# Kernel tuning notes

Hardware: AMD Instinct MI355X
Metric: run time of the kernel (lower is better)

The kernel has to match this reference:

```python
import jax, jax.numpy as jnp
import numpy as np

B = 8192      # env batch
M = 16        # n_machine
HID = 128     # machine_hidden_dim
HEADS = 1
BN_EPS = 1e-5


def _gat(h, gat_W, gat_a):
    # h: (B2, 2, HID); gat_W: (HID, HEADS*HID); gat_a: (HEADS, 2*HID, 1)
    B2 = h.shape[0]
    Wh = (h @ gat_W).reshape(B2, 2, HEADS, HID).transpose(0, 2, 1, 3)  # (B2,H,2,hid)
    src = jnp.einsum('bhnf,hfo->bhno', Wh, gat_a[:, :HID, :])   # (B2,H,2,1)
    tgt = jnp.einsum('bhnf,hfo->bhno', Wh, gat_a[:, HID:, :])   # (B2,H,2,1)
    e = jax.nn.leaky_relu(src + jnp.swapaxes(tgt, -1, -2), negative_slope=0.2)  # (B2,H,2,2)
    # static adjacency: row0 attends to both nodes, row1 only to itself (2->1 directed)
    adj = jnp.array([[1.0, 1.0], [0.0, 1.0]], dtype=e.dtype)
    e = jnp.where(adj > 0, e, jnp.asarray(-9e15, e.dtype))
    att = jax.nn.softmax(e, axis=-1)
    h_prime = att @ Wh                 # (B2,H,2,hid)
    return h_prime.mean(axis=1)        # concat=False -> mean over heads -> (B2,2,hid)


def setup_inputs() -> dict:
    key = jax.random.key(0)
    ks = jax.random.split(key, 24)
    s = 0.05
    inp = {
        'machine_fea_1': jax.random.normal(ks[0], (B, M, 6), jnp.float32),
        'machine_fea_2': jax.random.normal(ks[1], (B, M, 8), jnp.float32),
        'h_pooled_o': jax.random.normal(ks[2], (B, HID), jnp.float32),
        'machine_mask': jnp.zeros((B, 1, M), dtype=bool),
        # params (Linear weights stored as (in, out); original Linears have bias=False for feature projections)
        'W1': jax.random.normal(ks[3], (6, HID), jnp.float32) * s,
        'W2': jax.random.normal(ks[4], (8, HID), jnp.float32) * s,
        'gat_W': jax.random.normal(ks[5], (HID, HEADS * HID), jnp.float32) * s,
        'gat_a': jax.random.normal(ks[6], (HEADS, 2 * HID, 1), jnp.float32) * s,
        'bn_gamma': jnp.ones((HID,), jnp.float32),
        'bn_beta': jnp.zeros((HID,), jnp.float32),
        # MLPActor: 3 layers, in=3*HID, hidden=HID, out=1 (tanh hidden, linear out)
        'Wa1': jax.random.normal(ks[7], (3 * HID, HID), jnp.float32) * s,
        'ba1': jnp.zeros((HID,), jnp.float32),
        'Wa2': jax.random.normal(ks[8], (HID, HID), jnp.float32) * s,
        'ba2': jnp.zeros((HID,), jnp.float32),
        'Wa3': jax.random.normal(ks[9], (HID, 1), jnp.float32) * s,
        'ba3': jnp.zeros((1,), jnp.float32),
        # MLPCritic: 3 layers, in=HID, hidden=HID, out=2
        'Wc1': jax.random.normal(ks[10], (HID, HID), jnp.float32) * s,
        'bc1': jnp.zeros((HID,), jnp.float32),
        'Wc2': jax.random.normal(ks[11], (HID, HID), jnp.float32) * s,
        'bc2': jnp.zeros((HID,), jnp.float32),
        'Wc3': jax.random.normal(ks[12], (HID, 2), jnp.float32) * s,
        'bc3': jnp.zeros((2,), jnp.float32),
    }
    return inp


def reference(machine_fea_1, machine_fea_2, h_pooled_o, machine_mask,
              W1, W2, gat_W, gat_a, bn_gamma, bn_beta,
              Wa1, ba1, Wa2, ba2, Wa3, ba3,
              Wc1, bc1, Wc2, bc2, Wc3, bc3):
    m_fea1 = machine_fea_1 @ W1                       # (B,M,HID)
    m_fea2 = machine_fea_2 @ W2                       # (B,M,HID)
    # pair the two projections per machine node: (B*M, 2, HID)
    h12 = jnp.stack([m_fea1.reshape(-1, HID), m_fea2.reshape(-1, HID)], axis=1)
    g = jax.nn.elu(_gat(h12, gat_W, gat_a))
    g = jax.nn.elu(_gat(g, gat_W, gat_a))
    g = _gat(g, gat_W, gat_a)
    # NOTE: h_machine_feas is computed but unused downstream in the original forward (ablation)
    h_machine_feas = g.mean(axis=-2).reshape(-1, M, HID)
    # BatchNorm1d in training mode over flattened (B*M, HID)
    flat = m_fea1.reshape(-1, HID)
    mu = flat.mean(axis=0)
    var = flat.var(axis=0)  # biased, as torch BN uses for normalization
    h_m_nodes = (((flat - mu) / jnp.sqrt(var + BN_EPS)) * bn_gamma + bn_beta).reshape(-1, M, HID)
    h_pooled = h_m_nodes.mean(axis=1)                 # (B,HID)
    concat = jnp.concatenate([
        h_m_nodes,
        jnp.broadcast_to(h_pooled[:, None, :], h_m_nodes.shape),
        jnp.broadcast_to(h_pooled_o[:, None, :], h_m_nodes.shape),
    ], axis=-1)                                       # (B,M,3*HID)
    x = jnp.tanh(concat @ Wa1 + ba1)
    x = jnp.tanh(x @ Wa2 + ba2)
    mch_scores = (x @ Wa3 + ba3).squeeze(-1) * 10.0   # (B,M)
    mask = machine_mask.squeeze(1)
    mch_scores = jnp.where(mask, -jnp.inf, mch_scores)
    mch_prob = jax.nn.softmax(mch_scores, axis=-1)
    v = jnp.tanh(h_pooled @ Wc1 + bc1)
    v = jnp.tanh(v @ Wc2 + bc2)
    machine_v = v @ Wc3 + bc3                         # (B,2)
    return (mch_prob, h_pooled, machine_v)
```

## Files before the change

### kernel.cpp

```cpp
#include <hip/hip_runtime.h>
#include <hip/hip_bf16.h>
#include <math.h>

#define HID    128
#define BATCH  8192
#define NM     16
#define NROWS  (BATCH * NM)
#define BN_EPS 1e-5f

#define S1_BLOCKS   256
#define S1_ROWS     (NROWS / S1_BLOCKS)
#define PREP_BLOCKS 32
#define TOT_BLOCKS  (S1_BLOCKS + PREP_BLOCKS)

#define WS_PART  0
#define WS_SCALE 8192
#define WS_SHIFT 8320
#define WS_M1    8448
#define WS_SV    9216
#define WS_N1    9344
#define WS_CV    10112
#define WS_BW    10240

#define O1 ((size_t)BATCH * NM)
#define O2 (O1 + (size_t)BATCH * HID)

#define G    4
#define ROWS (G * NM)
#define LDH  136
#define ZLD  136
#define LDV  132

typedef __attribute__((ext_vector_type(8))) short short8_t;
typedef __attribute__((ext_vector_type(4))) float f32x4;

#define MFMA16(a, b, c) __builtin_amdgcn_mfma_f32_16x16x32_bf16(a, b, c, 0, 0, 0)

__device__ __forceinline__ unsigned short f2bf(float x) {
    __hip_bfloat16 h = __float2bfloat16(x);
    return *reinterpret_cast<unsigned short*>(&h);
}
__device__ __forceinline__ float bf2f(unsigned short u) {
    __hip_bfloat16 h = *reinterpret_cast<__hip_bfloat16*>(&u);
    return __bfloat162float(h);
}
__device__ __forceinline__ float ftanh(float x) {
    float e = __expf(2.0f * x);
    return 1.0f - 2.0f / (e + 1.0f);
}

__global__ __launch_bounds__(512) void stats_prep_kernel(
    const float* __restrict__ fea1,
    const float* __restrict__ Wa1, const float* __restrict__ Wa2,
    const float* __restrict__ Wc2,
    float* __restrict__ ws, unsigned short* __restrict__ wbt)
{
    const int tid = threadIdx.x;
    const int blk = blockIdx.x;

    if (blk >= S1_BLOCKS) {
        const int idx = (blk - S1_BLOCKS) * 512 + tid;
        const int k = idx >> 7, c = idx & 127;
        wbt[c * 128 + k]         = f2bf(Wa1[idx]);
        wbt[16384 + c * 128 + k] = f2bf(Wa2[idx]);
        wbt[32768 + c * 128 + k] = f2bf(Wa1[32768 + idx]);
        wbt[49152 + c * 128 + k] = f2bf(Wc2[idx]);
        return;
    }

    __shared__ float feaS[S1_ROWS * 6];
    __shared__ float redM[8 * 27];

    const float* src = fea1 + (size_t)blk * (S1_ROWS * 6);
    for (int i = tid; i < S1_ROWS * 6; i += 512) feaS[i] = src[i];
    __syncthreads();

    float f[6];
    #pragma unroll
    for (int j = 0; j < 6; ++j) f[j] = feaS[tid * 6 + j];

    float acc[27];
    #pragma unroll
    for (int j = 0; j < 6; ++j) acc[j] = f[j];
    {
        int idx = 6;
        #pragma unroll
        for (int j = 0; j < 6; ++j)
            #pragma unroll
            for (int k = j; k < 6; ++k) acc[idx++] = f[j] * f[k];
    }
    #pragma unroll
    for (int j = 0; j < 27; ++j) {
        acc[j] += __shfl_xor(acc[j], 1);
        acc[j] += __shfl_xor(acc[j], 2);
        acc[j] += __shfl_xor(acc[j], 4);
        acc[j] += __shfl_xor(acc[j], 8);
        acc[j] += __shfl_xor(acc[j], 16);
        acc[j] += __shfl_xor(acc[j], 32);
    }
    const int wv = tid >> 6;
    if ((tid & 63) == 0) {
        #pragma unroll
        for (int j = 0; j < 27; ++j) redM[wv * 27 + j] = acc[j];
    }
    __syncthreads();
    if (tid < 27) {
        float s = 0.f;
        #pragma unroll
        for (int w2 = 0; w2 < 8; ++w2) s += redM[w2 * 27 + tid];
        ws[WS_PART + blk * 32 + tid] = s;
    }
}

__global__ __launch_bounds__(512) void finalize_kernel(
    const float* __restrict__ W1,  const float* __restrict__ Wa1,
    const float* __restrict__ Wc1, const float* __restrict__ bc1,
    const float* __restrict__ gamma, const float* __restrict__ beta,
    float* __restrict__ ws, unsigned short* __restrict__ wbt)
{
    __shared__ float stageA[128 * 128];
    __shared__ float stageC[128 * 128];
    __shared__ double momS[27];
    __shared__ float scS2[HID], shS[HID];
    __shared__ float w1sS[6 * HID];

    const int tid = threadIdx.x;

    for (int i = tid; i < 128 * 128; i += 512) {
        stageA[i] = Wa1[16384 + i];
        stageC[i] = Wc1[i];
    }

    {
        const int j = tid >> 4;
        const int l = tid & 15;
        double s = 0.0;
        if (j < 27)
            for (int p = l; p < S1_BLOCKS; p += 16)
                s += (double)ws[WS_PART + p * 32 + j];
        s += __shfl_xor(s, 1);
        s += __shfl_xor(s, 2);
        s += __shfl_xor(s, 4);
        s += __shfl_xor(s, 8);
        if (j < 27 && l == 0) momS[j] = s;
    }
    __syncthreads();

    if (tid < 128) {
        float wv[6];
        #pragma unroll
        for (int j = 0; j < 6; ++j) wv[j] = W1[j * HID + tid];
        double sum = 0.0, ssq = 0.0;
        #pragma unroll
        for (int j = 0; j < 6; ++j) sum += (double)wv[j] * momS[j];
        {
            int idx = 6;
            #pragma unroll
            for (int j = 0; j < 6; ++j)
                #pragma unroll
                for (int k = j; k < 6; ++k) {
                    double t = (double)wv[j] * (double)wv[k] * momS[idx++];
                    ssq += (j == k) ? t : 2.0 * t;
                }
        }
        const double inv = 1.0 / (double)NROWS;
        double mu  = sum * inv;
        double var = ssq * inv - mu * mu;
        float sc = gamma[tid] * rsqrtf((float)var + BN_EPS);
        float sh = beta[tid] - (float)mu * sc;
        ws[WS_SCALE + tid] = sc;
        ws[WS_SHIFT + tid] = sh;
        scS2[tid] = sc;
        shS[tid]  = sh;
    }
    __syncthreads();
    for (int i = tid; i < 6 * HID; i += 512)
        w1sS[i] = W1[i] * scS2[i & 127];
    __syncthreads();

    if (tid < 256) {
        const int cc = tid & 127;
        const float* st = (tid < 128) ? stageA : stageC;
        float a[7] = {0.f, 0.f, 0.f, 0.f, 0.f, 0.f, 0.f};
        for (int k = 0; k < HID; ++k) {
            const float sv = st[k * 128 + cc];
            #pragma unroll
            for (int j = 0; j < 6; ++j)
                a[j] += w1sS[j * HID + k] * sv;
            a[6] += shS[k] * sv;
        }
        if (tid < 128) {
            #pragma unroll
            for (int j = 0; j < 6; ++j) ws[WS_M1 + j * HID + cc] = a[j];
            ws[WS_SV + cc] = a[6];
        } else {
            #pragma unroll
            for (int j = 0; j < 6; ++j) ws[WS_N1 + j * HID + cc] = a[j];
            ws[WS_CV + cc] = a[6] + bc1[cc];
        }
    }

    for (int idx = tid; idx < HID * 32; idx += 512) {
        const int col = idx >> 5, k = idx & 31;
        unsigned short v = 0;
        int kr = -1; bool lo = false;
        if (k < 6)                    kr = k;
        else if (k >= 8  && k < 14)   kr = k - 8;
        else if (k >= 16 && k < 22) { kr = k - 16; lo = true; }
        if (kr >= 0) {
            const float wv = w1sS[kr * HID + col];
            const unsigned short hi = f2bf(wv);
            v = lo ? f2bf(wv - bf2f(hi)) : hi;
        }
        wbt[65536 + col * 32 + k] = v;
    }
}

__global__ __launch_bounds__(256, 4) void main_kernel(
    const float* __restrict__ fea1, const float* __restrict__ hpo,
    const unsigned char* __restrict__ mask,
    const float* __restrict__ W1,
    const float* __restrict__ ba1, const float* __restrict__ ba2,
    const float* __restrict__ Wa3, const float* __restrict__ ba3,
    const float* __restrict__ bc2,
    const float* __restrict__ Wc3, const float* __restrict__ bc3,
    const float* __restrict__ ws, const unsigned short* __restrict__ wbt,
    float* __restrict__ out)
{
    __shared__ __align__(16) unsigned short hmS[ROWS * LDH];
    __shared__ __align__(16) unsigned short x1S[ROWS * LDH];
    __shared__ __align__(16) unsigned short zS[G * ZLD];
    __shared__ __align__(16) unsigned short v1bS[4 * LDV];
    __shared__ __align__(16) unsigned short v2bS[4 * LDV];
    __shared__ float scS[4 * ROWS];
    __shared__ float fmS[4][8];

    float* feaS = (float*)x1S;

    const int tid = threadIdx.x;
    const int b0  = blockIdx.x * G;

    const int w    = tid >> 6;
    const int lane = tid & 63;
    const int lr   = lane & 15;
    const int lg   = lane >> 4;
    const int n0   = 2 * w;

    const unsigned short* wbt1  = wbt;
    const unsigned short* wbt2  = wbt + 16384;
    const unsigned short* wbtB  = wbt + 32768;
    const unsigned short* wbtC2 = wbt + 49152;
    const unsigned short* wbtW1 = wbt + 65536;

    for (int i = tid; i < ROWS * 6; i += 256) feaS[i] = fea1[(size_t)b0 * (NM * 6) + i];
    for (int i = tid; i < G * HID; i += 256) {
        const int g = i >> 7, cc = i & 127;
        zS[g * ZLD + cc] = f2bf(hpo[(size_t)b0 * HID + i]);
    }

    short8_t bW[2];
    #pragma unroll
    for (int t = 0; t < 2; ++t)
        bW[t] = *(const short8_t*)(wbtW1 + ((n0 + t) * 16 + lr) * 32 + lg * 8);
    short8_t b1f[2][4];
    #pragma unroll
    for (int t = 0; t < 2; ++t) {
        const unsigned short* br = wbt1 + ((n0 + t) * 16 + lr) * 128 + lg * 8;
        #pragma unroll
        for (int kk = 0; kk < 4; ++kk) b1f[t][kk] = *(const short8_t*)(br + kk * 32);
    }
    const float sh0 = ws[WS_SHIFT + n0 * 16 + lr];
    const float sh1 = ws[WS_SHIFT + (n0 + 1) * 16 + lr];
    __syncthreads();

    #pragma unroll
    for (int g = 0; g < 4; ++g) {
        const float* fr = feaS + (g * 16 + lr) * 6;
        short8_t af;
        #pragma unroll
        for (int j = 0; j < 6; ++j) {
            const float x = fr[j];
            const unsigned short hx = f2bf(x);
            const unsigned short lx = f2bf(x - bf2f(hx));
            unsigned short sel = (lg == 1) ? lx : hx;
            if (lg == 3) sel = 0;
            af[j] = (short)sel;
        }
        af[6] = 0; af[7] = 0;

        #pragma unroll
        for (int t = 0; t < 2; ++t) {
            const float sh = t ? sh1 : sh0;
            f32x4 acc = {sh, sh, sh, sh};
            acc = MFMA16(af, bW[t], acc);
            #pragma unroll
            for (int i = 0; i < 4; ++i)
                hmS[(g * 16 + lg * 4 + i) * LDH + (n0 + t) * 16 + lr] = f2bf(acc[i]);
        }
    }
    if (tid < 24) {
        const int g = tid / 6, j = tid % 6;
        float s = 0.f;
        for (int m = 0; m < NM; ++m) s += feaS[(g * 16 + m) * 6 + j];
        fmS[g][j] = s * (1.0f / NM);
    }
    __syncthreads();

    f32x4 accB[2];
    {
        short8_t bBf[2][4];
        #pragma unroll
        for (int t = 0; t < 2; ++t) {
            const unsigned short* br = wbtB + ((n0 + t) * 16 + lr) * 128 + lg * 8;
            #pragma unroll
            for (int kk = 0; kk < 4; ++kk) bBf[t][kk] = *(const short8_t*)(br + kk * 32);
        }
        short8_t za[4];
        const unsigned short* zr = zS + (lr & 3) * ZLD + lg * 8;
        #pragma unroll
        for (int kk = 0; kk < 4; ++kk) za[kk] = *(const short8_t*)(zr + kk * 32);

        float fm[4][6];
        #pragma unroll
        for (int g = 0; g < 4; ++g)
            #pragma unroll
            for (int j = 0; j < 6; ++j) fm[g][j] = fmS[g][j];

        #pragma unroll
        for (int t = 0; t < 2; ++t) {
            const int col = (n0 + t) * 16 + lr;
            const float bias = ba1[col] + ws[WS_SV + col];
            float b_[4];
            #pragma unroll
            for (int g = 0; g < 4; ++g) {
                float a = bias;
                #pragma unroll
                for (int j = 0; j < 6; ++j) a += fm[g][j] * ws[WS_M1 + j * HID + col];
                b_[g] = a;
            }
            f32x4 acc = {b_[0], b_[1], b_[2], b_[3]};
            acc = MFMA16(za[0], bBf[t][0], acc);
            acc = MFMA16(za[1], bBf[t][1], acc);
            acc = MFMA16(za[2], bBf[t][2], acc);
            acc = MFMA16(za[3], bBf[t][3], acc);
            accB[t] = acc;
        }

        #pragma unroll
        for (int t = 0; t < 2; ++t) {
            const int col = (n0 + t) * 16 + lr;
            float a = ws[WS_CV + col];
            #pragma unroll
            for (int j = 0; j < 6; ++j) a += fm[lg][j] * ws[WS_N1 + j * HID + col];
            v1bS[lg * LDV + col] = f2bf(ftanh(a));
        }

        #pragma unroll
        for (int t = 0; t < 2; ++t) {
            const int col = (n0 + t) * 16 + lr;
            float a = 0.f;
            #pragma unroll
            for (int j = 0; j < 6; ++j) a += fm[lg][j] * W1[j * HID + col];
            a = a * ws[WS_SCALE + col] + ws[WS_SHIFT + col];
            out[O1 + (size_t)(b0 + lg) * HID + col] = a;
        }
    }

    short8_t b2f[2][4];
    #pragma unroll
    for (int t = 0; t < 2; ++t) {
        const unsigned short* br = wbt2 + ((n0 + t) * 16 + lr) * 128 + lg * 8;
        #pragma unroll
        for (int kk = 0; kk < 4; ++kk) b2f[t][kk] = *(const short8_t*)(br + kk * 32);
    }

    #pragma unroll
    for (int g = 0; g < 4; ++g) {
        short8_t ha[4];
        const unsigned short* ar = hmS + (g * 16 + lr) * LDH + lg * 8;
        #pragma unroll
        for (int kk = 0; kk < 4; ++kk) ha[kk] = *(const short8_t*)(ar + kk * 32);
        #pragma unroll
        for (int t = 0; t < 2; ++t) {
            const float bz = accB[t][g];
            f32x4 acc = {bz, bz, bz, bz};
            acc = MFMA16(ha[0], b1f[t][0], acc);
            acc = MFMA16(ha[1], b1f[t][1], acc);
            acc = MFMA16(ha[2], b1f[t][2], acc);
            acc = MFMA16(ha[3], b1f[t][3], acc);
            #pragma unroll
            for (int i = 0; i < 4; ++i)
                x1S[(g * 16 + lg * 4 + i) * LDH + (n0 + t) * 16 + lr] = f2bf(ftanh(acc[i]));
        }
    }
    __syncthreads();

    {
        short8_t va[4];
        const unsigned short* vr = v1bS + (lr & 3) * LDV + lg * 8;
        #pragma unroll
        for (int kk = 0; kk < 4; ++kk) va[kk] = *(const short8_t*)(vr + kk * 32);
        #pragma unroll
        for (int t = 0; t < 2; ++t) {
            const int n = n0 + t;
            const unsigned short* br = wbtC2 + (n * 16 + lr) * 128 + lg * 8;
            const float bi = bc2[n * 16 + lr];
            f32x4 acc = {bi, bi, bi, bi};
            acc = MFMA16(va[0], *(const short8_t*)(br),      acc);
            acc = MFMA16(va[1], *(const short8_t*)(br + 32), acc);
            acc = MFMA16(va[2], *(const short8_t*)(br + 64), acc);
            acc = MFMA16(va[3], *(const short8_t*)(br + 96), acc);
            if (lg == 0) {
                #pragma unroll
                for (int i = 0; i < 4; ++i)
                    v2bS[i * LDV + n * 16 + lr] = f2bf(ftanh(acc[i]));
            }
        }

        float p[4][4];
        #pragma unroll
        for (int g = 0; g < 4; ++g)
            #pragma unroll
            for (int i = 0; i < 4; ++i) p[g][i] = 0.f;

        const float wv0 = Wa3[n0 * 16 + lr];
        const float wv1 = Wa3[(n0 + 1) * 16 + lr];
        const float bi0 = ba2[n0 * 16 + lr];
        const float bi1 = ba2[(n0 + 1) * 16 + lr];
        #pragma unroll
        for (int g = 0; g < 4; ++g) {
            short8_t ha[4];
            const unsigned short* ar = x1S + (g * 16 + lr) * LDH + lg * 8;
            #pragma unroll
            for (int kk = 0; kk < 4; ++kk) ha[kk] = *(const short8_t*)(ar + kk * 32);
            #pragma unroll
            for (int t = 0; t < 2; ++t) {
                const float bi = t ? bi1 : bi0;
                f32x4 acc = {bi, bi, bi, bi};
                acc = MFMA16(ha[0], b2f[t][0], acc);
                acc = MFMA16(ha[1], b2f[t][1], acc);
                acc = MFMA16(ha[2], b2f[t][2], acc);
                acc = MFMA16(ha[3], b2f[t][3], acc);
                const float wv = t ? wv1 : wv0;
                #pragma unroll
                for (int i = 0; i < 4; ++i)
                    p[g][i] += ftanh(acc[i]) * wv;
            }
        }
        #pragma unroll
        for (int g = 0; g < 4; ++g) {
            #pragma unroll
            for (int i = 0; i < 4; ++i) {
                float v = p[g][i];
                v += __shfl_xor(v, 1);
                v += __shfl_xor(v, 2);
                v += __shfl_xor(v, 4);
                v += __shfl_xor(v, 8);
                if (lr == 0) scS[w * ROWS + g * 16 + lg * 4 + i] = v;
            }
        }
    }
    __syncthreads();

    {
        const int g = w;
        float s = scS[0 * ROWS + g * 16 + lr] + scS[1 * ROWS + g * 16 + lr]
                + scS[2 * ROWS + g * 16 + lr] + scS[3 * ROWS + g * 16 + lr];
        s = (s + ba3[0]) * 10.0f;
        if (mask[(size_t)(b0 + g) * NM + lr]) s = -INFINITY;
        float mx = s;
        mx = fmaxf(mx, __shfl_xor(mx, 1));
        mx = fmaxf(mx, __shfl_xor(mx, 2));
        mx = fmaxf(mx, __shfl_xor(mx, 4));
        mx = fmaxf(mx, __shfl_xor(mx, 8));
        float e = __expf(s - mx);
        float sum = e;
        sum += __shfl_xor(sum, 1);
        sum += __shfl_xor(sum, 2);
        sum += __shfl_xor(sum, 4);
        sum += __shfl_xor(sum, 8);
        if (lane < NM)
            out[(size_t)(b0 + g) * NM + lr] = e / sum;
    }

    {
        const int g = w;
        const int k2 = lane * 2;
        float v0 = bf2f(v2bS[g * LDV + k2]);
        float v1 = bf2f(v2bS[g * LDV + k2 + 1]);
        float4 wc = *(const float4*)(Wc3 + k2 * 2);
        float p0 = v0 * wc.x + v1 * wc.z;
        float p1 = v0 * wc.y + v1 * wc.w;
        p0 += __shfl_xor(p0, 1);  p1 += __shfl_xor(p1, 1);
        p0 += __shfl_xor(p0, 2);  p1 += __shfl_xor(p1, 2);
        p0 += __shfl_xor(p0, 4);  p1 += __shfl_xor(p1, 4);
        p0 += __shfl_xor(p0, 8);  p1 += __shfl_xor(p1, 8);
        p0 += __shfl_xor(p0, 16); p1 += __shfl_xor(p1, 16);
        p0 += __shfl_xor(p0, 32); p1 += __shfl_xor(p1, 32);
        if (lane == 0) {
            out[O2 + (size_t)(b0 + g) * 2 + 0] = p0 + bc3[0];
            out[O2 + (size_t)(b0 + g) * 2 + 1] = p1 + bc3[1];
        }
    }
}

extern "C" void kernel_launch(void* const* d_in, const int* in_sizes, int n_in,
                              void* d_out, int out_size, void* d_ws, size_t ws_size,
                              hipStream_t stream)
{
    const float* fea1  = (const float*)d_in[0];
    const float* hpo   = (const float*)d_in[2];
    const unsigned char* mask = (const unsigned char*)d_in[3];
    const float* W1    = (const float*)d_in[4];
    const float* gamma = (const float*)d_in[8];
    const float* beta  = (const float*)d_in[9];
    const float* Wa1   = (const float*)d_in[10];
    const float* ba1   = (const float*)d_in[11];
    const float* Wa2   = (const float*)d_in[12];
    const float* ba2   = (const float*)d_in[13];
    const float* Wa3   = (const float*)d_in[14];
    const float* ba3   = (const float*)d_in[15];
    const float* Wc1   = (const float*)d_in[16];
    const float* bc1   = (const float*)d_in[17];
    const float* Wc2   = (const float*)d_in[18];
    const float* bc2   = (const float*)d_in[19];
    const float* Wc3   = (const float*)d_in[20];
    const float* bc3   = (const float*)d_in[21];

    float* ws = (float*)d_ws;
    unsigned short* wbt = (unsigned short*)(ws + WS_BW);
    float* out = (float*)d_out;

    stats_prep_kernel<<<TOT_BLOCKS, 512, 0, stream>>>(
        fea1, Wa1, Wa2, Wc2, ws, wbt);
    finalize_kernel<<<1, 512, 0, stream>>>(
        W1, Wa1, Wc1, bc1, gamma, beta, ws, wbt);
    main_kernel<<<BATCH / G, 256, 0, stream>>>(
        fea1, hpo, mask, W1, ba1, ba2, Wa3, ba3,
        bc2, Wc3, bc3, ws, wbt, out);
}
```

Measured before the change: 73.67 us.

## Split finalize kernel across three blocks with K-split weight folding

The single-block finalize kernel becomes three blocks. Block 0 folds the BN scale into the Wa1 slice, block 1 folds it into Wc1, and block 2 builds the bf16 W1 tile. The weight folding now reads global memory directly and splits the K dimension over four thread groups, with partial sums reduced in shared memory, so the large 128KB shared staging buffers and the idle threads are gone. The cost is that every block redoes the moment reduction and BN statistics.

```diff
diff --git a/kernel.cpp b/kernel.cpp
--- a/kernel.cpp
+++ b/kernel.cpp
@@ -118,18 +118,13 @@
     const float* __restrict__ gamma, const float* __restrict__ beta,
     float* __restrict__ ws, unsigned short* __restrict__ wbt)
 {
-    __shared__ float stageA[128 * 128];
-    __shared__ float stageC[128 * 128];
     __shared__ double momS[27];
     __shared__ float scS2[HID], shS[HID];
     __shared__ float w1sS[6 * HID];
+    __shared__ float partS[4 * 7 * HID];
 
     const int tid = threadIdx.x;
-
-    for (int i = tid; i < 128 * 128; i += 512) {
-        stageA[i] = Wa1[16384 + i];
-        stageC[i] = Wc1[i];
-    }
+    const int blk = blockIdx.x;
 
     {
         const int j = tid >> 4;
@@ -168,51 +163,68 @@
         double var = ssq * inv - mu * mu;
         float sc = gamma[tid] * rsqrtf((float)var + BN_EPS);
         float sh = beta[tid] - (float)mu * sc;
-        ws[WS_SCALE + tid] = sc;
-        ws[WS_SHIFT + tid] = sh;
         scS2[tid] = sc;
         shS[tid]  = sh;
+        if (blk == 0) {
+            ws[WS_SCALE + tid] = sc;
+            ws[WS_SHIFT + tid] = sh;
+        }
     }
     __syncthreads();
     for (int i = tid; i < 6 * HID; i += 512)
         w1sS[i] = W1[i] * scS2[i & 127];
     __syncthreads();
 
-    if (tid < 256) {
+    if (blk == 2) {
+        for (int idx = tid; idx < HID * 32; idx += 512) {
+            const int col = idx >> 5, k = idx & 31;
+            unsigned short v = 0;
+            int kr = -1; bool lo = false;
+            if (k < 6)                    kr = k;
+            else if (k >= 8  && k < 14)   kr = k - 8;
+            else if (k >= 16 && k < 22) { kr = k - 16; lo = true; }
+            if (kr >= 0) {
+                const float wv = w1sS[kr * HID + col];
+                const unsigned short hi = f2bf(wv);
+                v = lo ? f2bf(wv - bf2f(hi)) : hi;
+            }
+            wbt[65536 + col * 32 + k] = v;
+        }
+        return;
+    }
+
+    {
+        const float* st = (blk == 0) ? (Wa1 + 16384) : Wc1;
         const int cc = tid & 127;
-        const float* st = (tid < 128) ? stageA : stageC;
+        const int kq = tid >> 7;
         float a[7] = {0.f, 0.f, 0.f, 0.f, 0.f, 0.f, 0.f};
-        for (int k = 0; k < HID; ++k) {
+        for (int k = kq * 32; k < kq * 32 + 32; ++k) {
             const float sv = st[k * 128 + cc];
             #pragma unroll
             for (int j = 0; j < 6; ++j)
                 a[j] += w1sS[j * HID + k] * sv;
             a[6] += shS[k] * sv;
         }
-        if (tid < 128) {
-            #pragma unroll
-            for (int j = 0; j < 6; ++j) ws[WS_M1 + j * HID + cc] = a[j];
-            ws[WS_SV + cc] = a[6];
-        } else {
-            #pragma unroll
-            for (int j = 0; j < 6; ++j) ws[WS_N1 + j * HID + cc] = a[j];
-            ws[WS_CV + cc] = a[6] + bc1[cc];
-        }
-    }
-
-    for (int idx = tid; idx < HID * 32; idx += 512) {
-        const int col = idx >> 5, k = idx & 31;
-        unsigned short v = 0;
-        int kr = -1; bool lo = false;
-        if (k < 6)                    kr = k;
-        else if (k >= 8  && k < 14)   kr = k - 8;
-        else if (k >= 16 && k < 22) { kr = k - 16; lo = true; }
-        if (kr >= 0) {
-            const float wv = w1sS[kr * HID + col];
-            const unsigned short hi = f2bf(wv);
-            v = lo ? f2bf(wv - bf2f(hi)) : hi;
-        }
-        wbt[65536 + col * 32 + k] = v;
+        #pragma unroll
+        for (int j = 0; j < 7; ++j)
+            partS[(kq * 7 + j) * HID + cc] = a[j];
+    }
+    __syncthreads();
+    if (tid < 128) {
+        #pragma unroll
+        for (int j = 0; j < 7; ++j) {
+            const float v = partS[(0 * 7 + j) * HID + tid]
+                          + partS[(1 * 7 + j) * HID + tid]
+                          + partS[(2 * 7 + j) * HID + tid]
+                          + partS[(3 * 7 + j) * HID + tid];
+            if (blk == 0) {
+                if (j < 6) ws[WS_M1 + j * HID + tid] = v;
+                else       ws[WS_SV + tid] = v;
+            } else {
+                if (j < 6) ws[WS_N1 + j * HID + tid] = v;
+                else       ws[WS_CV + tid] = v + bc1[tid];
+            }
+        }
     }
 }
 
@@ -533,7 +545,7 @@
 
     stats_prep_kernel<<<TOT_BLOCKS, 512, 0, stream>>>(
         fea1, Wa1, Wa2, Wc2, ws, wbt);
-    finalize_kernel<<<1, 512, 0, stream>>>(
+    finalize_kernel<<<3, 512, 0, stream>>>(
         W1, Wa1, Wc1, bc1, gamma, beta, ws, wbt);
     main_kernel<<<BATCH / G, 256, 0, stream>>>(
         fea1, hpo, mask, W1, ba1, ba2, Wa3, ba3,
```

Measured after the change: 68.66 us (median of 2 runs). 1.07x faster.
